# Optimization experiments

Hardware: AMD Instinct MI355X
Metric: run time of the kernel (lower is better)

## Reference

```python
import jax, jax.numpy as jnp
import numpy as np

MARGIN = 0.2
EPS = 1e-8
N, D_EMB, N_CLASSES = 8192, 256, 512


def setup_inputs() -> dict:
    key = jax.random.key(0)
    k1, k2 = jax.random.split(key)
    embeddings = jax.random.normal(k1, (N, D_EMB), dtype=jnp.float32)
    labels = jax.random.randint(k2, (N,), 0, N_CLASSES, dtype=jnp.int64)
    return {"embeddings": embeddings, "labels": labels}


def reference(embeddings, labels):
    # OnlineTripleLoss.forward with sampling_strategy='fixed_semi_hard', cosine metric.
    n = embeddings.shape[0]
    norms = jnp.linalg.norm(embeddings, axis=1, keepdims=True)
    xn = embeddings / jnp.maximum(norms, EPS)
    dist = 1.0 - xn @ xn.T                       # [N, N] cosine distance

    same = labels[:, None] == labels[None, :]    # same-label mask
    neg_mask = ~same
    has_neg = jnp.any(neg_mask, axis=1)          # anchor has at least one negative

    # fixed_semi_hard argmax(ap+margin-an) == argmin(an); fallback is also argmin(an)
    BIG = jnp.float32(1e9)
    dmin_neg = jnp.min(jnp.where(neg_mask, dist, BIG), axis=1)  # [N]

    # all anchor-positive combinations: same label, a < p (itertools.combinations order)
    upper = jnp.triu(jnp.ones((n, n), dtype=bool), 1)
    pair_mask = same & upper & has_neg[:, None]

    losses = jnp.maximum(dist - dmin_neg[:, None] + MARGIN, 0.0)
    count = jnp.sum(pair_mask)
    loss_sum = jnp.sum(jnp.where(pair_mask, losses, 0.0))
    loss = jnp.where(count > 0, loss_sum / jnp.maximum(count, 1).astype(jnp.float32), 0.0)
    return loss, count
```

## Files before the change

kernel.cpp:

```cpp
#include <hip/hip_runtime.h>
#include <hip/hip_bf16.h>

#define NROWS 8192
#define DEMB 256
#define MARGIN 0.2f
#define NCLS 512
#define TPC 8
#define NSTEP 16
#define MCAP 64
#define SROW 264

typedef __attribute__((ext_vector_type(4))) float f32x4;
typedef __attribute__((ext_vector_type(8))) short bf16x8;

static __device__ __forceinline__ unsigned short f2b(float f) {
    unsigned u = __builtin_bit_cast(unsigned, f);
    u += 0x7fffu + ((u >> 16) & 1u);
    return (unsigned short)(u >> 16);
}
static __device__ __forceinline__ float b2f(unsigned short b) {
    unsigned u = ((unsigned)b) << 16;
    return __builtin_bit_cast(float, u);
}
static __device__ __forceinline__ unsigned encf(float f) {
    unsigned u = __builtin_bit_cast(unsigned, f);
    return (u & 0x80000000u) ? ~u : (u | 0x80000000u);
}
static __device__ __forceinline__ float decf(unsigned e) {
    unsigned u = (e & 0x80000000u) ? (e ^ 0x80000000u) : ~e;
    return __builtin_bit_cast(float, u);
}
static __device__ __forceinline__ void gload16(const void* g, void* l) {
    __builtin_amdgcn_global_load_lds(
        (const __attribute__((address_space(1))) unsigned int*)g,
        (__attribute__((address_space(3))) unsigned int*)l, 16, 0, 0);
}

__global__ __launch_bounds__(256) void k_norm(const float* __restrict__ x,
                                              unsigned short* __restrict__ xnb,
                                              unsigned* __restrict__ amax,
                                              int* __restrict__ bcnt) {
    int gid = blockIdx.x * blockDim.x + threadIdx.x;
    if (gid < NROWS) amax[gid] = 0u;
    if (gid < NCLS) bcnt[gid] = 0;
    int row  = gid >> 6;
    int lane = threadIdx.x & 63;
    const float4* p = reinterpret_cast<const float4*>(x + (size_t)row * DEMB) + lane;
    float4 v = *p;
    float s = v.x * v.x + v.y * v.y + v.z * v.z + v.w * v.w;
#pragma unroll
    for (int m = 1; m < 64; m <<= 1) s += __shfl_xor(s, m);
    float inv = 1.0f / fmaxf(sqrtf(s), 1e-8f);
    ushort4 o;
    o.x = f2b(v.x * inv); o.y = f2b(v.y * inv);
    o.z = f2b(v.z * inv); o.w = f2b(v.w * inv);
    *(reinterpret_cast<ushort4*>(xnb + (size_t)row * DEMB) + lane) = o;
}

__global__ __launch_bounds__(256) void k_bucket(const int* __restrict__ labels,
                                                int* __restrict__ bcnt,
                                                int* __restrict__ mem) {
    int i = blockIdx.x * 256 + threadIdx.x;
    if (i < NROWS) {
        int l = labels[i];
        int slot = atomicAdd(&bcnt[l], 1);
        if (slot < MCAP) mem[l * MCAP + slot] = i;
    }
}

__global__ __launch_bounds__(512, 2) void k_maxneg(const unsigned short* __restrict__ xnb,
                                                   const int* __restrict__ labels,
                                                   unsigned* __restrict__ amax) {
    extern __shared__ char lds[];
    unsigned short* Bl = (unsigned short*)lds;

    int tid  = threadIdx.x;
    int wid  = tid >> 6, lane = tid & 63;
    int wr   = wid >> 1, wc = wid & 1;
    int arow = lane & 15, kgrp = lane >> 4;

    int i0 = blockIdx.x * 128;
    int j0 = blockIdx.y * (TPC * 128);

    bf16x8 a[2][8];
    const unsigned short* ap0 = xnb + (size_t)(i0 + wr * 32 + arow) * DEMB + kgrp * 8;
#pragma unroll
    for (int m = 0; m < 2; ++m)
#pragma unroll
        for (int kk = 0; kk < 8; ++kk)
            a[m][kk] = *(const bf16x8*)(ap0 + m * 16 * DEMB + kk * 32);

    int rlab[2][4];
#pragma unroll
    for (int m = 0; m < 2; ++m)
#pragma unroll
        for (int r = 0; r < 4; ++r)
            rlab[m][r] = labels[i0 + wr * 32 + m * 16 + kgrp * 4 + r];

    float rmax[2][4] = {{-1e30f, -1e30f, -1e30f, -1e30f},
                        {-1e30f, -1e30f, -1e30f, -1e30f}};
    f32x4 acc[2][4] = {};

    auto stage = [&](int buf, int t, int h) {
#pragma unroll
        for (int is = 0; is < 4; ++is) {
            int idx  = is * 512 + tid;
            int row  = idx >> 4;
            int colb = (idx & 15) << 4;
            int scol = (colb ^ ((row & 15) << 4)) >> 1;
            const unsigned short* src =
                xnb + (size_t)(j0 + t * 128 + row) * DEMB + h * 128 + scol;
            unsigned short* dst = Bl + buf * 16384 + is * 4096 + wid * 512;
            gload16(src, dst);
        }
    };

    int clab[4], nlab[4];
    stage(0, 0, 0);
#pragma unroll
    for (int n = 0; n < 4; ++n) clab[n] = labels[j0 + wc * 64 + n * 16 + arow];

    int sw = arow << 4;
    for (int s = 0; s < NSTEP; ++s) {
        __syncthreads();
        if (s + 1 < NSTEP) stage((s + 1) & 1, (s + 1) >> 1, (s + 1) & 1);
        int tile = s >> 1, h = s & 1;
        if (h == 0 && tile + 1 < TPC) {
#pragma unroll
            for (int n = 0; n < 4; ++n)
                nlab[n] = labels[j0 + (tile + 1) * 128 + wc * 64 + n * 16 + arow];
        }
        const char* Bt = (const char*)(Bl + (s & 1) * 16384);
        bf16x8 b[4][4];
#pragma unroll
        for (int n = 0; n < 4; ++n) {
            int rb = (wc * 64 + n * 16 + arow) * 256;
#pragma unroll
            for (int ksl = 0; ksl < 4; ++ksl)
                b[n][ksl] = *(const bf16x8*)(Bt + rb + ((ksl * 64 + kgrp * 16) ^ sw));
        }
#pragma unroll
        for (int m = 0; m < 2; ++m)
#pragma unroll
            for (int n = 0; n < 4; ++n)
#pragma unroll
                for (int ksl = 0; ksl < 4; ++ksl)
                    acc[m][n] = __builtin_amdgcn_mfma_f32_16x16x32_bf16(
                        a[m][h * 4 + ksl], b[n][ksl], acc[m][n], 0, 0, 0);
        if (h == 1) {
#pragma unroll
            for (int m = 0; m < 2; ++m)
#pragma unroll
                for (int r = 0; r < 4; ++r) {
                    float v = rmax[m][r];
                    int rl = rlab[m][r];
#pragma unroll
                    for (int n = 0; n < 4; ++n)
                        if (clab[n] != rl) v = fmaxf(v, acc[m][n][r]);
                    rmax[m][r] = v;
                }
#pragma unroll
            for (int m = 0; m < 2; ++m)
#pragma unroll
                for (int n = 0; n < 4; ++n) acc[m][n] = (f32x4){0.f, 0.f, 0.f, 0.f};
#pragma unroll
            for (int n = 0; n < 4; ++n) clab[n] = nlab[n];
        }
    }

    float* smax = (float*)Bl;
#pragma unroll
    for (int m = 0; m < 2; ++m)
#pragma unroll
        for (int r = 0; r < 4; ++r) {
            float v = rmax[m][r];
#pragma unroll
            for (int msk = 1; msk < 16; msk <<= 1) v = fmaxf(v, __shfl_xor(v, msk));
            if (arow == 0) smax[wc * 128 + wr * 32 + m * 16 + kgrp * 4 + r] = v;
        }
    __syncthreads();
    if (tid < 128) {
        float v = fmaxf(smax[tid], smax[128 + tid]);
        if (v > -1e29f) atomicMax(amax + i0 + tid, encf(v));
    }
}

__global__ __launch_bounds__(256) void k_cpairs2(const unsigned short* __restrict__ xnb,
                                                 const unsigned* __restrict__ amax,
                                                 const int* __restrict__ bcnt,
                                                 const int* __restrict__ mem,
                                                 float* __restrict__ closs,
                                                 int* __restrict__ ccnt) {
    __shared__ unsigned short srows[MCAP * SROW];
    __shared__ int mlist[MCAP];
    __shared__ float sdm[MCAP];
    __shared__ unsigned char shn[MCAP];
    __shared__ float slloss[16];
    __shared__ int slcnt[16];

    int c   = blockIdx.x;
    int tid = threadIdx.x;
    int nc  = bcnt[c];
    if (nc > MCAP) nc = MCAP;

    if (tid < nc) {
        int gi = mem[c * MCAP + tid];
        mlist[tid] = gi;
        unsigned e = amax[gi];
        shn[tid] = (e != 0u);
        sdm[tid] = 1.0f - decf(e);
    }
    __syncthreads();
    int nch = nc * 32;
    for (int ch = tid; ch < nch; ch += 256) {
        int r = ch >> 5, cc = ch & 31;
        *(bf16x8*)(srows + r * SROW + cc * 8) =
            *(const bf16x8*)(xnb + (size_t)mlist[r] * DEMB + cc * 8);
    }
    __syncthreads();

    int slot = tid >> 4, gl = tid & 15;
    int npairs = nc * (nc - 1) / 2;
    float gloss = 0.f;
    int gcnt = 0;
    for (int p = slot; p < npairs; p += 16) {
        int i = 0, rem = p;
        while (rem >= nc - 1 - i) { rem -= nc - 1 - i; ++i; }
        int j = i + 1 + rem;
        bf16x8 a0 = *(const bf16x8*)(srows + i * SROW + gl * 16);
        bf16x8 a1 = *(const bf16x8*)(srows + i * SROW + gl * 16 + 8);
        bf16x8 b0 = *(const bf16x8*)(srows + j * SROW + gl * 16);
        bf16x8 b1 = *(const bf16x8*)(srows + j * SROW + gl * 16 + 8);
        float dot = 0.f;
#pragma unroll
        for (int e = 0; e < 8; ++e) {
            dot += b2f((unsigned short)a0[e]) * b2f((unsigned short)b0[e]);
            dot += b2f((unsigned short)a1[e]) * b2f((unsigned short)b1[e]);
        }
#pragma unroll
        for (int msk = 1; msk < 16; msk <<= 1) dot += __shfl_xor(dot, msk);
        if (gl == 0) {
            int ai = (mlist[i] < mlist[j]) ? i : j;
            if (shn[ai]) {
                gloss += fmaxf(1.0f - dot - sdm[ai] + MARGIN, 0.0f);
                gcnt += 1;
            }
        }
    }
    if (gl == 0) { slloss[slot] = gloss; slcnt[slot] = gcnt; }
    __syncthreads();
    if (tid == 0) {
        float s = 0.f; int k = 0;
        for (int q = 0; q < 16; ++q) { s += slloss[q]; k += slcnt[q]; }
        closs[c] = s; ccnt[c] = k;
    }
}

__global__ __launch_bounds__(256) void k_final(const float* __restrict__ closs,
                                               const int* __restrict__ ccnt,
                                               float* __restrict__ out) {
    __shared__ float sl[256];
    __shared__ int   sc[256];
    int tid = threadIdx.x;
    float s = closs[tid] + closs[tid + 256];
    int   k = ccnt[tid] + ccnt[tid + 256];
    sl[tid] = s; sc[tid] = k;
    __syncthreads();
    for (int st = 128; st > 0; st >>= 1) {
        if (tid < st) {
            sl[tid] += sl[tid + st];
            sc[tid] += sc[tid + st];
        }
        __syncthreads();
    }
    if (tid == 0) {
        out[0] = (sc[0] > 0) ? sl[0] / (float)sc[0] : 0.0f;
        out[1] = (float)sc[0];
    }
}

extern "C" void kernel_launch(void* const* d_in, const int* in_sizes, int n_in,
                              void* d_out, int out_size, void* d_ws, size_t ws_size,
                              hipStream_t stream) {
    const float* emb  = (const float*)d_in[0];
    const int* labels = (const int*)d_in[1];
    float* out = (float*)d_out;

    char* ws = (char*)d_ws;
    unsigned short* xnb = (unsigned short*)ws;
    unsigned* amax = (unsigned*)(ws + (size_t)4 * 1024 * 1024);
    int* bcnt = (int*)(ws + (size_t)4 * 1024 * 1024 + 32768);
    int* mem  = (int*)(ws + (size_t)4 * 1024 * 1024 + 34816);
    float* closs = (float*)(ws + (size_t)4 * 1024 * 1024 + 34816 + 131072);
    int*   ccnt  = (int*)  (ws + (size_t)4 * 1024 * 1024 + 34816 + 131072 + 2048);

    k_norm<<<NROWS / 4, 256, 0, stream>>>(emb, xnb, amax, bcnt);
    k_bucket<<<NROWS / 256, 256, 0, stream>>>(labels, bcnt, mem);
    dim3 g2(NROWS / 128, NCLS / 64);
    k_maxneg<<<g2, 512, 65536, stream>>>(xnb, labels, amax);
    k_cpairs2<<<NCLS, 256, 0, stream>>>(xnb, amax, bcnt, mem, closs, ccnt);
    k_final<<<1, 256, 0, stream>>>(closs, ccnt, out);
}
```

Baseline: 80.13 us.

## Fold bucketing into norm kernel and final reduction into pair kernel

Bucketing by label moves into the normalisation kernel, with a memset replacing the in-kernel zeroing of counters. The final reduction kernel is replaced by global atomics and a last-block-done counter inside the pair kernel. The pair kernel also drops its LDS staging of class rows and reads bf16 rows directly from global/L2. Together these cut two kernel launches and the staging barriers, at the cost of an extra memset node, atomic contention and uncached global reads per pair.

```diff
diff --git a/kernel.cpp b/kernel.cpp
--- a/kernel.cpp
+++ b/kernel.cpp
@@ -8,7 +8,6 @@
 #define TPC 8
 #define NSTEP 16
 #define MCAP 64
-#define SROW 264
 
 typedef __attribute__((ext_vector_type(4))) float f32x4;
 typedef __attribute__((ext_vector_type(8))) short bf16x8;
@@ -37,12 +36,18 @@
 }
 
 __global__ __launch_bounds__(256) void k_norm(const float* __restrict__ x,
+                                              const int* __restrict__ labels,
                                               unsigned short* __restrict__ xnb,
                                               unsigned* __restrict__ amax,
-                                              int* __restrict__ bcnt) {
+                                              int* __restrict__ bcnt,
+                                              int* __restrict__ mem) {
     int gid = blockIdx.x * blockDim.x + threadIdx.x;
-    if (gid < NROWS) amax[gid] = 0u;
-    if (gid < NCLS) bcnt[gid] = 0;
+    if (gid < NROWS) {
+        amax[gid] = 0u;
+        int l = labels[gid];
+        int slot = atomicAdd(&bcnt[l], 1);
+        if (slot < MCAP) mem[l * MCAP + slot] = gid;
+    }
     int row  = gid >> 6;
     int lane = threadIdx.x & 63;
     const float4* p = reinterpret_cast<const float4*>(x + (size_t)row * DEMB) + lane;
@@ -55,17 +60,6 @@
     o.x = f2b(v.x * inv); o.y = f2b(v.y * inv);
     o.z = f2b(v.z * inv); o.w = f2b(v.w * inv);
     *(reinterpret_cast<ushort4*>(xnb + (size_t)row * DEMB) + lane) = o;
-}
-
-__global__ __launch_bounds__(256) void k_bucket(const int* __restrict__ labels,
-                                                int* __restrict__ bcnt,
-                                                int* __restrict__ mem) {
-    int i = blockIdx.x * 256 + threadIdx.x;
-    if (i < NROWS) {
-        int l = labels[i];
-        int slot = atomicAdd(&bcnt[l], 1);
-        if (slot < MCAP) mem[l * MCAP + slot] = i;
-    }
 }
 
 __global__ __launch_bounds__(512, 2) void k_maxneg(const unsigned short* __restrict__ xnb,
@@ -185,16 +179,14 @@
     }
 }
 
-__global__ __launch_bounds__(256) void k_cpairs2(const unsigned short* __restrict__ xnb,
+__global__ __launch_bounds__(256) void k_cpairs3(const unsigned short* __restrict__ xnb,
                                                  const unsigned* __restrict__ amax,
                                                  const int* __restrict__ bcnt,
                                                  const int* __restrict__ mem,
-                                                 float* __restrict__ closs,
-                                                 int* __restrict__ ccnt) {
-    __shared__ unsigned short srows[MCAP * SROW];
-    __shared__ int mlist[MCAP];
-    __shared__ float sdm[MCAP];
-    __shared__ unsigned char shn[MCAP];
+                                                 float* __restrict__ gsum,
+                                                 int* __restrict__ gcnt,
+                                                 unsigned* __restrict__ done,
+                                                 float* __restrict__ out) {
     __shared__ float slloss[16];
     __shared__ int slcnt[16];
 
@@ -202,35 +194,21 @@
     int tid = threadIdx.x;
     int nc  = bcnt[c];
     if (nc > MCAP) nc = MCAP;
-
-    if (tid < nc) {
-        int gi = mem[c * MCAP + tid];
-        mlist[tid] = gi;
-        unsigned e = amax[gi];
-        shn[tid] = (e != 0u);
-        sdm[tid] = 1.0f - decf(e);
-    }
-    __syncthreads();
-    int nch = nc * 32;
-    for (int ch = tid; ch < nch; ch += 256) {
-        int r = ch >> 5, cc = ch & 31;
-        *(bf16x8*)(srows + r * SROW + cc * 8) =
-            *(const bf16x8*)(xnb + (size_t)mlist[r] * DEMB + cc * 8);
-    }
-    __syncthreads();
+    const int* cm = mem + c * MCAP;
 
     int slot = tid >> 4, gl = tid & 15;
     int npairs = nc * (nc - 1) / 2;
     float gloss = 0.f;
-    int gcnt = 0;
+    int gc = 0;
     for (int p = slot; p < npairs; p += 16) {
         int i = 0, rem = p;
         while (rem >= nc - 1 - i) { rem -= nc - 1 - i; ++i; }
         int j = i + 1 + rem;
-        bf16x8 a0 = *(const bf16x8*)(srows + i * SROW + gl * 16);
-        bf16x8 a1 = *(const bf16x8*)(srows + i * SROW + gl * 16 + 8);
-        bf16x8 b0 = *(const bf16x8*)(srows + j * SROW + gl * 16);
-        bf16x8 b1 = *(const bf16x8*)(srows + j * SROW + gl * 16 + 8);
+        int gi = cm[i], gj = cm[j];
+        const bf16x8* ra = (const bf16x8*)(xnb + (size_t)gi * DEMB) + gl * 2;
+        const bf16x8* rb = (const bf16x8*)(xnb + (size_t)gj * DEMB) + gl * 2;
+        bf16x8 a0 = ra[0], a1 = ra[1];
+        bf16x8 b0 = rb[0], b1 = rb[1];
         float dot = 0.f;
 #pragma unroll
         for (int e = 0; e < 8; ++e) {
@@ -240,42 +218,30 @@
 #pragma unroll
         for (int msk = 1; msk < 16; msk <<= 1) dot += __shfl_xor(dot, msk);
         if (gl == 0) {
-            int ai = (mlist[i] < mlist[j]) ? i : j;
-            if (shn[ai]) {
-                gloss += fmaxf(1.0f - dot - sdm[ai] + MARGIN, 0.0f);
-                gcnt += 1;
+            int ga = (gi < gj) ? gi : gj;
+            unsigned e = amax[ga];
+            if (e != 0u) {
+                float sdm = 1.0f - decf(e);
+                gloss += fmaxf(1.0f - dot - sdm + MARGIN, 0.0f);
+                gc += 1;
             }
         }
     }
-    if (gl == 0) { slloss[slot] = gloss; slcnt[slot] = gcnt; }
+    if (gl == 0) { slloss[slot] = gloss; slcnt[slot] = gc; }
     __syncthreads();
     if (tid == 0) {
         float s = 0.f; int k = 0;
         for (int q = 0; q < 16; ++q) { s += slloss[q]; k += slcnt[q]; }
-        closs[c] = s; ccnt[c] = k;
-    }
-}
-
-__global__ __launch_bounds__(256) void k_final(const float* __restrict__ closs,
-                                               const int* __restrict__ ccnt,
-                                               float* __restrict__ out) {
-    __shared__ float sl[256];
-    __shared__ int   sc[256];
-    int tid = threadIdx.x;
-    float s = closs[tid] + closs[tid + 256];
-    int   k = ccnt[tid] + ccnt[tid + 256];
-    sl[tid] = s; sc[tid] = k;
-    __syncthreads();
-    for (int st = 128; st > 0; st >>= 1) {
-        if (tid < st) {
-            sl[tid] += sl[tid + st];
-            sc[tid] += sc[tid + st];
-        }
-        __syncthreads();
-    }
-    if (tid == 0) {
-        out[0] = (sc[0] > 0) ? sl[0] / (float)sc[0] : 0.0f;
-        out[1] = (float)sc[0];
+        atomicAdd(gsum, s);
+        atomicAdd(gcnt, k);
+        __threadfence();
+        unsigned old = atomicAdd(done, 1u);
+        if (old == NCLS - 1) {
+            float S = atomicAdd(gsum, 0.0f);
+            int   K = atomicAdd(gcnt, 0);
+            out[0] = (K > 0) ? S / (float)K : 0.0f;
+            out[1] = (float)K;
+        }
     }
 }
 
@@ -289,15 +255,15 @@
     char* ws = (char*)d_ws;
     unsigned short* xnb = (unsigned short*)ws;
     unsigned* amax = (unsigned*)(ws + (size_t)4 * 1024 * 1024);
-    int* bcnt = (int*)(ws + (size_t)4 * 1024 * 1024 + 32768);
-    int* mem  = (int*)(ws + (size_t)4 * 1024 * 1024 + 34816);
-    float* closs = (float*)(ws + (size_t)4 * 1024 * 1024 + 34816 + 131072);
-    int*   ccnt  = (int*)  (ws + (size_t)4 * 1024 * 1024 + 34816 + 131072 + 2048);
-
-    k_norm<<<NROWS / 4, 256, 0, stream>>>(emb, xnb, amax, bcnt);
-    k_bucket<<<NROWS / 256, 256, 0, stream>>>(labels, bcnt, mem);
+    int*      bcnt = (int*)     (ws + (size_t)4 * 1024 * 1024 + 32768);
+    float*    gsum = (float*)   (ws + (size_t)4 * 1024 * 1024 + 34816);
+    int*      gcnt = (int*)     (ws + (size_t)4 * 1024 * 1024 + 34820);
+    unsigned* done = (unsigned*)(ws + (size_t)4 * 1024 * 1024 + 34824);
+    int*      mem  = (int*)     (ws + (size_t)4 * 1024 * 1024 + 36864);
+
+    hipMemsetAsync(bcnt, 0, 2048 + 16, stream);
+    k_norm<<<NROWS / 4, 256, 0, stream>>>(emb, labels, xnb, amax, bcnt, mem);
     dim3 g2(NROWS / 128, NCLS / 64);
     k_maxneg<<<g2, 512, 65536, stream>>>(xnb, labels, amax);
-    k_cpairs2<<<NCLS, 256, 0, stream>>>(xnb, amax, bcnt, mem, closs, ccnt);
-    k_final<<<1, 256, 0, stream>>>(closs, ccnt, out);
-}
+    k_cpairs3<<<NCLS, 256, 0, stream>>>(xnb, amax, bcnt, mem, gsum, gcnt, done, out);
+}
```

Result: slower. 92.19 us (+15.1%).
